# Performance work log

Measured on AMD Instinct MI355X. Metric: run time of the kernel, lower is better.

Reference implementation:

```python
import jax, jax.numpy as jnp
import numpy as np

N = 8192          # total nodes in the batch of graphs
ATOM = 64         # atom_feats
HID = 128         # hidden_feats
HEADS = 8         # num_heads
NUM_GRAPHS = 256  # number of graphs (max value of `batch`)
NEG_SLOPE = 0.2   # LeakyReLU slope in GAT attention


def setup_inputs() -> dict:
    key = jax.random.key(0)
    ks = jax.random.split(key, 16)
    x = jax.random.normal(ks[0], (N, ATOM), dtype=jnp.float32)
    adj = (jax.random.uniform(ks[1], (N, N)) < 0.01).astype(jnp.float32)
    adj = jnp.maximum(adj, jnp.eye(N, dtype=jnp.float32))
    batch = jnp.sort(jax.random.randint(ks[2], (N,), 0, NUM_GRAPHS)).astype(jnp.int32)

    def u(k, shape, fan_in):
        lim = 1.0 / np.sqrt(fan_in)
        return jax.random.uniform(k, shape, jnp.float32, -lim, lim)

    in1 = HID * HEADS
    params = dict(
        W0=u(ks[3], (ATOM, HID), ATOM), a0_src=u(ks[4], (HID,), HID), a0_dst=u(ks[5], (HID,), HID),
        W1=u(ks[6], (in1, HID), in1), a1_src=u(ks[7], (HID,), HID), a1_dst=u(ks[8], (HID,), HID),
        W2=u(ks[9], (in1, HID), in1), a2_src=u(ks[10], (HID,), HID), a2_dst=u(ks[11], (HID,), HID),
        fc_w=u(ks[12], (HID, 1), HID), fc_b=u(ks[13], (1,), HID),
    )
    return dict(x=x, adj=adj, batch=batch, **params)


def _gat_layer(h_in, W, a_src, a_dst, mask):
    # standard dense GAT: Wh, e_ij = leakyrelu(a_src.Wh_i + a_dst.Wh_j), masked softmax, aggregate
    h = h_in @ W                                         # [N, HID]
    e = jax.nn.leaky_relu((h @ a_src)[:, None] + (h @ a_dst)[None, :], NEG_SLOPE)  # [N, N]
    e = jnp.where(mask, e, jnp.float32(-1e9))
    attn = jax.nn.softmax(e, axis=1)                     # [N, N]
    return attn @ h                                      # [N, HID]


def reference(x, adj, batch, W0, a0_src, a0_dst, W1, a1_src, a1_dst, W2, a2_src, a2_dst, fc_w, fc_b):
    # eval mode: dropout is identity. The torch module calls the SAME layer instance per head,
    # so concat of heads == tile, and the final stacked mean == a single layer call.
    mask = adj > 0
    h0 = _gat_layer(x, W0, a0_src, a0_dst, mask)
    x1 = jax.nn.relu(jnp.tile(h0, (1, HEADS)))           # [N, HID*HEADS]
    h1 = _gat_layer(x1, W1, a1_src, a1_dst, mask)
    x2 = jax.nn.relu(jnp.tile(h1, (1, HEADS)))
    h2 = _gat_layer(x2, W2, a2_src, a2_dst, mask)        # mean over identical heads == h2
    # global mean pool over graphs
    sums = jax.ops.segment_sum(h2, batch, num_segments=NUM_GRAPHS)           # [G, HID]
    cnt = jax.ops.segment_sum(jnp.ones((N, 1), h2.dtype), batch, num_segments=NUM_GRAPHS)
    pooled = sums / jnp.maximum(cnt, 1.0)
    out = pooled @ fc_w + fc_b                           # [G, 1]
    return out[:, 0]
```

## Files before the change

kernel.cpp:

```cpp
#include <hip/hip_runtime.h>
#include <cstdint>
#include <cstddef>

#define NN 8192
#define ATOMF 64
#define HID 128
#define HEADS 8
#define NG 256
#define ELLW 192
#define NEGSLOPE 0.2f

typedef unsigned long long u64;

__global__ __launch_bounds__(256, 4) void k_scan_ell(const float* __restrict__ adj,
                                                     int* __restrict__ ell,
                                                     int4* __restrict__ tb) {
    __shared__ u64 bml[4][128];
    int t = threadIdx.x, wid = t >> 6, l = t & 63;
    int row = blockIdx.x * 4 + wid;
    const float4* a4 = (const float4*)(adj + (size_t)row * NN);
    u64* bmr = bml[wid];
    #pragma unroll 8
    for (int s = 0; s < 32; ++s) {
        float4 v = a4[s * 64 + l];
        u64 b0 = __ballot(v.x > 0.f);
        u64 b1 = __ballot(v.y > 0.f);
        u64 b2 = __ballot(v.z > 0.f);
        u64 b3 = __ballot(v.w > 0.f);
        if (l < 4) bmr[s * 4 + l] = (l == 0) ? b0 : (l == 1) ? b1 : (l == 2) ? b2 : b3;
    }
    __syncthreads();
    u64 w0 = bmr[2 * l];
    u64 w1 = bmr[2 * l + 1];
    int c = __popcll(w0) + __popcll(w1);
    int incl = c;
    #pragma unroll
    for (int o = 1; o < 64; o <<= 1) {
        int u = __shfl_up(incl, o);
        if (l >= o) incl += u;
    }
    int pos = incl - c;
    int total = __shfl(incl, 63);
    int p16 = __shfl(incl, 15);
    int p32 = __shfl(incl, 31);
    int p48 = __shfl(incl, 47);
    if (l == 0) {
        int4 b;
        b.x = p16 < ELLW ? p16 : ELLW;
        b.y = p32 < ELLW ? p32 : ELLW;
        b.z = p48 < ELLW ? p48 : ELLW;
        b.w = total < ELLW ? total : ELLW;
        tb[row] = b;
    }
    int* er = ell + (size_t)row * ELLW;
    int gw0 = 2 * l, gw1 = 2 * l + 1;
    int base0 = (gw0 >> 2) * 256 + (gw0 & 3);
    int base1 = (gw1 >> 2) * 256 + (gw1 & 3);
    while (w0) {
        int bit = __builtin_ctzll(w0);
        w0 &= w0 - 1;
        if (pos < ELLW) er[pos++] = base0 + 4 * bit;
    }
    while (w1) {
        int bit = __builtin_ctzll(w1);
        w1 &= w1 - 1;
        if (pos < ELLW) er[pos++] = base1 + 4 * bit;
    }
}

__global__ __launch_bounds__(256) void k_front2(
    const float* __restrict__ x,
    const float* __restrict__ W0, const float* __restrict__ a0s, const float* __restrict__ a0d,
    const float* __restrict__ W1, const float* __restrict__ W2,
    float* __restrict__ Wr1, float* __restrict__ Wr2,
    float* __restrict__ g0, float* __restrict__ ssrc, float* __restrict__ sdst) {
    int b = blockIdx.x, t = threadIdx.x;
    if (b < 128) {
        const float* W = (b < 64) ? W1 : W2;
        float* Wr = (b < 64) ? Wr1 : Wr2;
        int i = (b & 63) * 256 + t;
        int k = i >> 7, cc = i & 127;
        float s = 0.f;
        #pragma unroll
        for (int h = 0; h < HEADS; ++h) s += W[(size_t)(h * HID + k) * HID + cc];
        Wr[i] = s;
    } else {
        __shared__ float Xl[32 * ATOMF];
        int row0 = (b - 128) * 32;
        const float4* Xg = (const float4*)(x + (size_t)row0 * ATOMF);
        float4* Xl4 = (float4*)Xl;
        #pragma unroll
        for (int i = t; i < 32 * ATOMF / 4; i += 256) Xl4[i] = Xg[i];
        __syncthreads();
        int cg = t & 31, rg = t >> 5;
        int c0 = cg * 4;
        float acc[4][4];
        #pragma unroll
        for (int r = 0; r < 4; ++r)
            #pragma unroll
            for (int c = 0; c < 4; ++c) acc[r][c] = 0.f;
        for (int k = 0; k < ATOMF; k += 4) {
            float4 w0 = *(const float4*)(W0 + (size_t)(k + 0) * HID + c0);
            float4 w1 = *(const float4*)(W0 + (size_t)(k + 1) * HID + c0);
            float4 w2 = *(const float4*)(W0 + (size_t)(k + 2) * HID + c0);
            float4 w3 = *(const float4*)(W0 + (size_t)(k + 3) * HID + c0);
            #pragma unroll
            for (int r = 0; r < 4; ++r) {
                float4 xv = *(const float4*)(&Xl[(rg * 4 + r) * ATOMF + k]);
                acc[r][0] += xv.x * w0.x + xv.y * w1.x + xv.z * w2.x + xv.w * w3.x;
                acc[r][1] += xv.x * w0.y + xv.y * w1.y + xv.z * w2.y + xv.w * w3.y;
                acc[r][2] += xv.x * w0.z + xv.y * w1.z + xv.z * w2.z + xv.w * w3.z;
                acc[r][3] += xv.x * w0.w + xv.y * w1.w + xv.z * w2.w + xv.w * w3.w;
            }
        }
        float4 asv = *(const float4*)(a0s + c0);
        float4 adv = *(const float4*)(a0d + c0);
        #pragma unroll
        for (int r = 0; r < 4; ++r) {
            int row = row0 + rg * 4 + r;
            *(float4*)(g0 + (size_t)row * HID + c0) =
                make_float4(acc[r][0], acc[r][1], acc[r][2], acc[r][3]);
            float ps = acc[r][0] * asv.x + acc[r][1] * asv.y + acc[r][2] * asv.z + acc[r][3] * asv.w;
            float pd = acc[r][0] * adv.x + acc[r][1] * adv.y + acc[r][2] * adv.z + acc[r][3] * adv.w;
            #pragma unroll
            for (int o = 16; o; o >>= 1) {
                ps += __shfl_xor(ps, o);
                pd += __shfl_xor(pd, o);
            }
            if (cg == 0) { ssrc[row] = ps; sdst[row] = pd; }
        }
    }
}

template<int DO_GEMM>
__global__ __launch_bounds__(256, 4) void k_layer(
    const float* __restrict__ g, const float* __restrict__ ssrc_in,
    const float* __restrict__ sdst_in,
    const int* __restrict__ ell, const int4* __restrict__ tb,
    const float* __restrict__ Wr, const float* __restrict__ as_,
    const float* __restrict__ ad_,
    float* __restrict__ gout, float* __restrict__ ssrc_out,
    float* __restrict__ sdst_out) {
    __shared__ float wls[4][ELLW];
    __shared__ int jls[4][ELLW];
    __shared__ float xls[4][HID];
    int wid = threadIdx.x >> 6, l = threadIdx.x & 63;
    int row = blockIdx.x * 4 + wid;
    float* wl = wls[wid];
    int* jl = jls[wid];
    int4 tbr = tb[row];
    int d = tbr.w;
    float si = ssrc_in[row];
    const int* er = ell + (size_t)row * ELLW;
    float m = -1e30f;
    for (int k = l; k < d; k += 64) {
        int j = er[k];
        float e = si + sdst_in[j];
        e = e > 0.f ? e : NEGSLOPE * e;
        jl[k] = j << 7;
        wl[k] = e;
        m = fmaxf(m, e);
    }
    #pragma unroll
    for (int o = 32; o; o >>= 1) m = fmaxf(m, __shfl_xor(m, o));
    float s = 0.f;
    for (int k = l; k < d; k += 64) {
        float w = __expf(wl[k] - m);
        wl[k] = w;
        s += w;
    }
    #pragma unroll
    for (int o = 32; o; o >>= 1) s += __shfl_xor(s, o);
    float inv = 1.f / s;
    int half = l >> 5;
    int d0 = (l & 31) * 4;
    const float* hd = g + d0;
    float4 acc = make_float4(0.f, 0.f, 0.f, 0.f);
    int bounds[4] = {tbr.x, tbr.y, tbr.z, tbr.w};
    int ka = 0;
    #pragma unroll
    for (int T = 0; T < 4; ++T) {
        int kb = bounds[T];
        int k = ka;
        for (; k + 8 <= kb; k += 8) {
            int j0 = jl[k + half],     j1 = jl[k + 2 + half];
            int j2 = jl[k + 4 + half], j3 = jl[k + 6 + half];
            float w0 = wl[k + half],     w1 = wl[k + 2 + half];
            float w2 = wl[k + 4 + half], w3 = wl[k + 6 + half];
            float4 v0 = *(const float4*)(hd + j0);
            float4 v1 = *(const float4*)(hd + j1);
            float4 v2 = *(const float4*)(hd + j2);
            float4 v3 = *(const float4*)(hd + j3);
            acc.x += w0 * v0.x; acc.y += w0 * v0.y; acc.z += w0 * v0.z; acc.w += w0 * v0.w;
            acc.x += w1 * v1.x; acc.y += w1 * v1.y; acc.z += w1 * v1.z; acc.w += w1 * v1.w;
            acc.x += w2 * v2.x; acc.y += w2 * v2.y; acc.z += w2 * v2.z; acc.w += w2 * v2.w;
            acc.x += w3 * v3.x; acc.y += w3 * v3.y; acc.z += w3 * v3.z; acc.w += w3 * v3.w;
        }
        for (; k + 2 <= kb; k += 2) {
            int j = jl[k + half];
            float w = wl[k + half];
            float4 v = *(const float4*)(hd + j);
            acc.x += w * v.x; acc.y += w * v.y; acc.z += w * v.z; acc.w += w * v.w;
        }
        if (k < kb && half == 0) {
            int j = jl[k];
            float w = wl[k];
            float4 v = *(const float4*)(hd + j);
            acc.x += w * v.x; acc.y += w * v.y; acc.z += w * v.z; acc.w += w * v.w;
        }
        ka = kb;
    }
    acc.x += __shfl_xor(acc.x, 32);
    acc.y += __shfl_xor(acc.y, 32);
    acc.z += __shfl_xor(acc.z, 32);
    acc.w += __shfl_xor(acc.w, 32);
    acc.x *= inv; acc.y *= inv; acc.z *= inv; acc.w *= inv;
    if (DO_GEMM == 0) {
        if (l < 32)
            *(float4*)(gout + (size_t)row * HID + d0) = acc;
        return;
    }
    float* xl = xls[wid];
    if (l < 32) {
        float4 r;
        r.x = fmaxf(acc.x, 0.f); r.y = fmaxf(acc.y, 0.f);
        r.z = fmaxf(acc.z, 0.f); r.w = fmaxf(acc.w, 0.f);
        *(float4*)(xl + d0) = r;
    }
    float acc0 = 0.f, acc1 = 0.f;
    for (int kk = 0; kk < HID; kk += 4) {
        float4 xv = *(const float4*)(&xl[kk]);
        float wa0 = Wr[(size_t)(kk + 0) * HID + l];
        float wb0 = Wr[(size_t)(kk + 0) * HID + l + 64];
        float wa1 = Wr[(size_t)(kk + 1) * HID + l];
        float wb1 = Wr[(size_t)(kk + 1) * HID + l + 64];
        float wa2 = Wr[(size_t)(kk + 2) * HID + l];
        float wb2 = Wr[(size_t)(kk + 2) * HID + l + 64];
        float wa3 = Wr[(size_t)(kk + 3) * HID + l];
        float wb3 = Wr[(size_t)(kk + 3) * HID + l + 64];
        acc0 += xv.x * wa0 + xv.y * wa1 + xv.z * wa2 + xv.w * wa3;
        acc1 += xv.x * wb0 + xv.y * wb1 + xv.z * wb2 + xv.w * wb3;
    }
    gout[(size_t)row * HID + l]      = acc0;
    gout[(size_t)row * HID + l + 64] = acc1;
    float ps = acc0 * as_[l] + acc1 * as_[l + 64];
    float pd = acc0 * ad_[l] + acc1 * ad_[l + 64];
    #pragma unroll
    for (int o = 32; o; o >>= 1) {
        ps += __shfl_xor(ps, o);
        pd += __shfl_xor(pd, o);
    }
    if (l == 0) { ssrc_out[row] = ps; sdst_out[row] = pd; }
}

__global__ __launch_bounds__(256) void k_poolfc(const float* __restrict__ h,
                                                const int* __restrict__ batch,
                                                const float* __restrict__ fcw,
                                                const float* __restrict__ fcb,
                                                float* __restrict__ out) {
    int wid = threadIdx.x >> 6, l = threadIdx.x & 63;
    int g = blockIdx.x * 4 + wid;
    int lo = 0, hi = NN;
    while (lo < hi) { int mid = (lo + hi) >> 1; if (batch[mid] < g) lo = mid + 1; else hi = mid; }
    int e0 = lo;
    hi = NN;
    while (lo < hi) { int mid = (lo + hi) >> 1; if (batch[mid] <= g) lo = mid + 1; else hi = mid; }
    int e1 = lo;
    float sum = 0.f;
    for (int r = e0; r < e1; ++r) {
        const float* hr = h + (size_t)r * HID;
        sum += hr[l] * fcw[l] + hr[l + 64] * fcw[l + 64];
    }
    #pragma unroll
    for (int o = 32; o; o >>= 1) sum += __shfl_xor(sum, o);
    if (l == 0) out[g] = sum / fmaxf((float)(e1 - e0), 1.f) + fcb[0];
}

extern "C" void kernel_launch(void* const* d_in, const int* in_sizes, int n_in,
                              void* d_out, int out_size, void* d_ws, size_t ws_size,
                              hipStream_t stream) {
    const float* x    = (const float*)d_in[0];
    const float* adj  = (const float*)d_in[1];
    const int*   batch= (const int*)  d_in[2];
    const float* W0   = (const float*)d_in[3];
    const float* a0s  = (const float*)d_in[4];
    const float* a0d  = (const float*)d_in[5];
    const float* W1   = (const float*)d_in[6];
    const float* a1s  = (const float*)d_in[7];
    const float* a1d  = (const float*)d_in[8];
    const float* W2   = (const float*)d_in[9];
    const float* a2s  = (const float*)d_in[10];
    const float* a2d  = (const float*)d_in[11];
    const float* fcw  = (const float*)d_in[12];
    const float* fcb  = (const float*)d_in[13];
    float* out = (float*)d_out;

    char* ws = (char*)d_ws;
    size_t off = 0;
    auto alloc = [&](size_t bytes) {
        char* p = ws + off;
        off = (off + bytes + 255) & ~255UL;
        return p;
    };
    int*   ell  = (int*)  alloc((size_t)NN * ELLW * 4);
    int4*  tb   = (int4*) alloc((size_t)NN * 16);
    float* hA   = (float*)alloc((size_t)NN * HID * 4);
    float* hB   = (float*)alloc((size_t)NN * HID * 4);
    float* sAs  = (float*)alloc((size_t)NN * 4);
    float* sAd  = (float*)alloc((size_t)NN * 4);
    float* sBs  = (float*)alloc((size_t)NN * 4);
    float* sBd  = (float*)alloc((size_t)NN * 4);
    float* Wr1  = (float*)alloc((size_t)HID * HID * 4);
    float* Wr2  = (float*)alloc((size_t)HID * HID * 4);
    (void)ws_size; (void)in_sizes; (void)n_in; (void)out_size;

    k_scan_ell<<<NN / 4, 256, 0, stream>>>(adj, ell, tb);
    k_front2<<<128 + 256, 256, 0, stream>>>(x, W0, a0s, a0d, W1, W2,
                                            Wr1, Wr2, hA, sAs, sAd);
    k_layer<1><<<NN / 4, 256, 0, stream>>>(hA, sAs, sAd, ell, tb, Wr1, a1s, a1d,
                                           hB, sBs, sBd);
    k_layer<1><<<NN / 4, 256, 0, stream>>>(hB, sBs, sBd, ell, tb, Wr2, a2s, a2d,
                                           hA, sAs, sAd);
    k_layer<0><<<NN / 4, 256, 0, stream>>>(hA, sAs, sAd, ell, tb, nullptr, nullptr,
                                           nullptr, hB, nullptr, nullptr);
    k_poolfc<<<NG / 4, 256, 0, stream>>>(hB, batch, fcw, fcb, out);
}
```

Baseline: 176.8 us.

## Split each GAT row across two wavefronts and drop max-subtraction in softmax

Each row's neighbour aggregation and the follow-on 128x128 GEMM are now split across two wavefronts instead of one, with partial sums combined through shared memory and block barriers. The grid doubles to keep all rows covered. The softmax no longer subtracts the row maximum, removing one pass and a reduction, at the risk of exp overflow for large logits. The tile-bounds ordering from tb (x,y,z) is dropped in favour of a simple halved range with zero-padded entries, and more barriers are added per block.

New measurement: 176.4 us. No clear change (-0.2%).

```diff
diff --git a/kernel.cpp b/kernel.cpp
--- a/kernel.cpp
+++ b/kernel.cpp
@@ -141,116 +141,116 @@
     const float* __restrict__ ad_,
     float* __restrict__ gout, float* __restrict__ ssrc_out,
     float* __restrict__ sdst_out) {
-    __shared__ float wls[4][ELLW];
-    __shared__ int jls[4][ELLW];
-    __shared__ float xls[4][HID];
-    int wid = threadIdx.x >> 6, l = threadIdx.x & 63;
-    int row = blockIdx.x * 4 + wid;
-    float* wl = wls[wid];
-    int* jl = jls[wid];
-    int4 tbr = tb[row];
-    int d = tbr.w;
+    __shared__ float wls[2][ELLW + 2];
+    __shared__ int   jls[2][ELLW + 2];
+    __shared__ float xls[2][HID];
+    __shared__ float pacc[2][2][HID];
+    __shared__ float pden[2][2];
+    __shared__ float psc[2][2][2];
+    int t = threadIdx.x, wid = t >> 6, l = t & 63;
+    int row2 = wid >> 1, wh = wid & 1;
+    int row = blockIdx.x * 2 + row2;
+    float* wl = wls[row2];
+    int* jl = jls[row2];
+    int d = tb[row].w;
     float si = ssrc_in[row];
     const int* er = ell + (size_t)row * ELLW;
-    float m = -1e30f;
-    for (int k = l; k < d; k += 64) {
+    float s = 0.f;
+    for (int k = wh * 64 + l; k < d; k += 128) {
         int j = er[k];
         float e = si + sdst_in[j];
         e = e > 0.f ? e : NEGSLOPE * e;
+        float w = __expf(e);
         jl[k] = j << 7;
-        wl[k] = e;
-        m = fmaxf(m, e);
-    }
-    #pragma unroll
-    for (int o = 32; o; o >>= 1) m = fmaxf(m, __shfl_xor(m, o));
-    float s = 0.f;
-    for (int k = l; k < d; k += 64) {
-        float w = __expf(wl[k] - m);
         wl[k] = w;
         s += w;
     }
     #pragma unroll
     for (int o = 32; o; o >>= 1) s += __shfl_xor(s, o);
-    float inv = 1.f / s;
+    if (l == 0) pden[row2][wh] = s;
+    if (wh == 0 && l == 0) { wl[d] = 0.f; jl[d] = 0; wl[d + 1] = 0.f; jl[d + 1] = 0; }
+    __syncthreads();
+    float inv = 1.f / (pden[row2][0] + pden[row2][1]);
+    int dpad = (d + 1) & ~1;
+    int dh = ((dpad >> 1) + 1) & ~1;
+    if (dh > dpad) dh = dpad;
+    int ka = wh ? dh : 0;
+    int kb = wh ? dpad : dh;
     int half = l >> 5;
     int d0 = (l & 31) * 4;
     const float* hd = g + d0;
     float4 acc = make_float4(0.f, 0.f, 0.f, 0.f);
-    int bounds[4] = {tbr.x, tbr.y, tbr.z, tbr.w};
-    int ka = 0;
-    #pragma unroll
-    for (int T = 0; T < 4; ++T) {
-        int kb = bounds[T];
-        int k = ka;
-        for (; k + 8 <= kb; k += 8) {
-            int j0 = jl[k + half],     j1 = jl[k + 2 + half];
-            int j2 = jl[k + 4 + half], j3 = jl[k + 6 + half];
-            float w0 = wl[k + half],     w1 = wl[k + 2 + half];
-            float w2 = wl[k + 4 + half], w3 = wl[k + 6 + half];
-            float4 v0 = *(const float4*)(hd + j0);
-            float4 v1 = *(const float4*)(hd + j1);
-            float4 v2 = *(const float4*)(hd + j2);
-            float4 v3 = *(const float4*)(hd + j3);
-            acc.x += w0 * v0.x; acc.y += w0 * v0.y; acc.z += w0 * v0.z; acc.w += w0 * v0.w;
-            acc.x += w1 * v1.x; acc.y += w1 * v1.y; acc.z += w1 * v1.z; acc.w += w1 * v1.w;
-            acc.x += w2 * v2.x; acc.y += w2 * v2.y; acc.z += w2 * v2.z; acc.w += w2 * v2.w;
-            acc.x += w3 * v3.x; acc.y += w3 * v3.y; acc.z += w3 * v3.z; acc.w += w3 * v3.w;
-        }
-        for (; k + 2 <= kb; k += 2) {
-            int j = jl[k + half];
-            float w = wl[k + half];
-            float4 v = *(const float4*)(hd + j);
-            acc.x += w * v.x; acc.y += w * v.y; acc.z += w * v.z; acc.w += w * v.w;
-        }
-        if (k < kb && half == 0) {
-            int j = jl[k];
-            float w = wl[k];
-            float4 v = *(const float4*)(hd + j);
-            acc.x += w * v.x; acc.y += w * v.y; acc.z += w * v.z; acc.w += w * v.w;
-        }
-        ka = kb;
+    int k = ka;
+    for (; k + 8 <= kb; k += 8) {
+        int j0 = jl[k + half],     j1 = jl[k + 2 + half];
+        int j2 = jl[k + 4 + half], j3 = jl[k + 6 + half];
+        float w0 = wl[k + half],     w1 = wl[k + 2 + half];
+        float w2 = wl[k + 4 + half], w3 = wl[k + 6 + half];
+        float4 v0 = *(const float4*)(hd + j0);
+        float4 v1 = *(const float4*)(hd + j1);
+        float4 v2 = *(const float4*)(hd + j2);
+        float4 v3 = *(const float4*)(hd + j3);
+        acc.x += w0 * v0.x; acc.y += w0 * v0.y; acc.z += w0 * v0.z; acc.w += w0 * v0.w;
+        acc.x += w1 * v1.x; acc.y += w1 * v1.y; acc.z += w1 * v1.z; acc.w += w1 * v1.w;
+        acc.x += w2 * v2.x; acc.y += w2 * v2.y; acc.z += w2 * v2.z; acc.w += w2 * v2.w;
+        acc.x += w3 * v3.x; acc.y += w3 * v3.y; acc.z += w3 * v3.z; acc.w += w3 * v3.w;
+    }
+    for (; k < kb; k += 2) {
+        int j = jl[k + half];
+        float w = wl[k + half];
+        float4 v = *(const float4*)(hd + j);
+        acc.x += w * v.x; acc.y += w * v.y; acc.z += w * v.z; acc.w += w * v.w;
     }
     acc.x += __shfl_xor(acc.x, 32);
     acc.y += __shfl_xor(acc.y, 32);
     acc.z += __shfl_xor(acc.z, 32);
     acc.w += __shfl_xor(acc.w, 32);
-    acc.x *= inv; acc.y *= inv; acc.z *= inv; acc.w *= inv;
+    if (l < 32) *(float4*)(&pacc[row2][wh][d0]) = acc;
+    __syncthreads();
+    float4 tot = make_float4(0.f, 0.f, 0.f, 0.f);
+    if (l < 32) {
+        float4 a0 = *(const float4*)(&pacc[row2][0][d0]);
+        float4 a1 = *(const float4*)(&pacc[row2][1][d0]);
+        tot.x = (a0.x + a1.x) * inv;
+        tot.y = (a0.y + a1.y) * inv;
+        tot.z = (a0.z + a1.z) * inv;
+        tot.w = (a0.w + a1.w) * inv;
+    }
     if (DO_GEMM == 0) {
-        if (l < 32)
-            *(float4*)(gout + (size_t)row * HID + d0) = acc;
+        if (wh == 0 && l < 32)
+            *(float4*)(gout + (size_t)row * HID + d0) = tot;
         return;
     }
-    float* xl = xls[wid];
-    if (l < 32) {
+    if (wh == 0 && l < 32) {
         float4 r;
-        r.x = fmaxf(acc.x, 0.f); r.y = fmaxf(acc.y, 0.f);
-        r.z = fmaxf(acc.z, 0.f); r.w = fmaxf(acc.w, 0.f);
-        *(float4*)(xl + d0) = r;
-    }
-    float acc0 = 0.f, acc1 = 0.f;
+        r.x = fmaxf(tot.x, 0.f); r.y = fmaxf(tot.y, 0.f);
+        r.z = fmaxf(tot.z, 0.f); r.w = fmaxf(tot.w, 0.f);
+        *(float4*)(&xls[row2][d0]) = r;
+    }
+    __syncthreads();
+    int col = l + wh * 64;
+    float accc = 0.f;
     for (int kk = 0; kk < HID; kk += 4) {
-        float4 xv = *(const float4*)(&xl[kk]);
-        float wa0 = Wr[(size_t)(kk + 0) * HID + l];
-        float wb0 = Wr[(size_t)(kk + 0) * HID + l + 64];
-        float wa1 = Wr[(size_t)(kk + 1) * HID + l];
-        float wb1 = Wr[(size_t)(kk + 1) * HID + l + 64];
-        float wa2 = Wr[(size_t)(kk + 2) * HID + l];
-        float wb2 = Wr[(size_t)(kk + 2) * HID + l + 64];
-        float wa3 = Wr[(size_t)(kk + 3) * HID + l];
-        float wb3 = Wr[(size_t)(kk + 3) * HID + l + 64];
-        acc0 += xv.x * wa0 + xv.y * wa1 + xv.z * wa2 + xv.w * wa3;
-        acc1 += xv.x * wb0 + xv.y * wb1 + xv.z * wb2 + xv.w * wb3;
-    }
-    gout[(size_t)row * HID + l]      = acc0;
-    gout[(size_t)row * HID + l + 64] = acc1;
-    float ps = acc0 * as_[l] + acc1 * as_[l + 64];
-    float pd = acc0 * ad_[l] + acc1 * ad_[l + 64];
+        float4 xv = *(const float4*)(&xls[row2][kk]);
+        accc += xv.x * Wr[(size_t)(kk + 0) * HID + col]
+              + xv.y * Wr[(size_t)(kk + 1) * HID + col]
+              + xv.z * Wr[(size_t)(kk + 2) * HID + col]
+              + xv.w * Wr[(size_t)(kk + 3) * HID + col];
+    }
+    gout[(size_t)row * HID + col] = accc;
+    float ps = accc * as_[col];
+    float pd = accc * ad_[col];
     #pragma unroll
     for (int o = 32; o; o >>= 1) {
         ps += __shfl_xor(ps, o);
         pd += __shfl_xor(pd, o);
     }
-    if (l == 0) { ssrc_out[row] = ps; sdst_out[row] = pd; }
+    if (l == 0) { psc[row2][wh][0] = ps; psc[row2][wh][1] = pd; }
+    __syncthreads();
+    if (wh == 0 && l == 0) {
+        ssrc_out[row] = psc[row2][0][0] + psc[row2][1][0];
+        sdst_out[row] = psc[row2][0][1] + psc[row2][1][1];
+    }
 }
 
 __global__ __launch_bounds__(256) void k_poolfc(const float* __restrict__ h,
@@ -317,11 +317,11 @@
     k_scan_ell<<<NN / 4, 256, 0, stream>>>(adj, ell, tb);
     k_front2<<<128 + 256, 256, 0, stream>>>(x, W0, a0s, a0d, W1, W2,
                                             Wr1, Wr2, hA, sAs, sAd);
-    k_layer<1><<<NN / 4, 256, 0, stream>>>(hA, sAs, sAd, ell, tb, Wr1, a1s, a1d,
+    k_layer<1><<<NN / 2, 256, 0, stream>>>(hA, sAs, sAd, ell, tb, Wr1, a1s, a1d,
                                            hB, sBs, sBd);
-    k_layer<1><<<NN / 4, 256, 0, stream>>>(hB, sBs, sBd, ell, tb, Wr2, a2s, a2d,
+    k_layer<1><<<NN / 2, 256, 0, stream>>>(hB, sBs, sBd, ell, tb, Wr2, a2s, a2d,
                                            hA, sAs, sAd);
-    k_layer<0><<<NN / 4, 256, 0, stream>>>(hA, sAs, sAd, ell, tb, nullptr, nullptr,
+    k_layer<0><<<NN / 2, 256, 0, stream>>>(hA, sAs, sAd, ell, tb, nullptr, nullptr,
                                            nullptr, hB, nullptr, nullptr);
     k_poolfc<<<NG / 4, 256, 0, stream>>>(hB, batch, fcw, fcb, out);
 }
```
